# Optimization experiments

Measured on AMD Instinct MI355X. Metric: run time of the kernel, lower is better.

Reference implementation:

```python
import jax, jax.numpy as jnp
import numpy as np

OUT_H, OUT_W = 7, 7  # out_size from init_kwargs


def _split_coefficient(size, k):
    # Matches __split_coefficient: equal bins of round(size/k), last absorbs remainder.
    u = int(round(size / k))
    s = [u] * k
    s[-1] += size - k * u
    return s


def setup_inputs() -> dict:
    key = jax.random.key(0)
    x = jax.random.normal(key, (128, 57, 57, 512), dtype=jnp.float32)
    return {"x": x}


def reference(x) -> jnp.ndarray:
    # Adaptive max pooling over irregular static bins (NHWC -> [N, 7, 7, C]).
    N, H, W, C = x.shape
    h_s = _split_coefficient(H, OUT_H)
    w_s = _split_coefficient(W, OUT_W)
    h_off = np.cumsum([0] + h_s)  # static bin boundaries
    w_off = np.cumsum([0] + w_s)
    # Max over each H bin -> [N, OUT_H, W, C]
    rows = [x[:, h_off[i]:h_off[i + 1]].max(axis=1, keepdims=True) for i in range(OUT_H)]
    xh = jnp.concatenate(rows, axis=1)
    # Max over each W bin -> [N, OUT_H, OUT_W, C]
    cols = [xh[:, :, w_off[j]:w_off[j + 1]].max(axis=2, keepdims=True) for j in range(OUT_W)]
    return jnp.concatenate(cols, axis=2)
```

## Files before the change

### kernel.cpp

```cpp
#include <hip/hip_runtime.h>


#define N_  128
#define H_  57
#define W_  57
#define C_  512
#define OH_ 7
#define OW_ 7
#define C4_ (C_ / 4)

__global__ __launch_bounds__(128)
void adaptive_maxpool_kernel(const float* __restrict__ x, float* __restrict__ out) {
    const int bid = blockIdx.x;
    const int ow  = bid % OW_;
    const int oh  = (bid / OW_) % OH_;
    const int n   = bid / (OW_ * OH_);
    const int c4  = threadIdx.x;

    const int h0 = oh * 8;
    const int h1 = (oh == OH_ - 1) ? H_ : h0 + 8;
    const int w0 = ow * 8;
    const int w1 = (ow == OW_ - 1) ? W_ : w0 + 8;

    const float4* __restrict__ xin =
        reinterpret_cast<const float4*>(x) + (size_t)n * H_ * W_ * C4_ + c4;

    float4 m = make_float4(-INFINITY, -INFINITY, -INFINITY, -INFINITY);
    for (int h = h0; h < h1; ++h) {
        const float4* row = xin + (size_t)h * W_ * C4_ + (size_t)w0 * C4_;
        #pragma unroll 4
        for (int w = w0; w < w1; ++w) {
            float4 v = *row;
            row += C4_;
            m.x = fmaxf(m.x, v.x);
            m.y = fmaxf(m.y, v.y);
            m.z = fmaxf(m.z, v.z);
            m.w = fmaxf(m.w, v.w);
        }
    }

    float4* o = reinterpret_cast<float4*>(out) + (size_t)bid * C4_ + c4;
    *o = m;
}

extern "C" void kernel_launch(void* const* d_in, const int* in_sizes, int n_in,
                              void* d_out, int out_size, void* d_ws, size_t ws_size,
                              hipStream_t stream) {
    const float* x = (const float*)d_in[0];
    float* out = (float*)d_out;
    const int grid = N_ * OH_ * OW_;
    adaptive_maxpool_kernel<<<grid, 128, 0, stream>>>(x, out);
}
```

Measured before the change: 161.8 us.

## Process full width strip per block with split-row threads and LDS reduction

Each block now handles one (n, oh) row strip across all seven output columns instead of one output cell. The 256 threads form two groups that split the strip's rows in half, and the partial maxima are combined through shared memory before the output is written. Every thread issues a fully unrolled set of loads across the width, which raises memory-level parallelism per thread and cuts the block count by seven. The cost is more registers (seven float4 accumulators), a barrier, and fewer, larger blocks, which could limit occupancy.

```diff
diff --git a/kernel.cpp b/kernel.cpp
--- a/kernel.cpp
+++ b/kernel.cpp
@@ -1,46 +1,73 @@
 #include <hip/hip_runtime.h>
 
 
-#define N_  128
-#define H_  57
-#define W_  57
-#define C_  512
-#define OH_ 7
-#define OW_ 7
-#define C4_ (C_ / 4)
+#define N_   128
+#define H_   57
+#define W_   57
+#define C_   512
+#define OH_  7
+#define OW_  7
+#define C4_  (C_ / 4)
 
-__global__ __launch_bounds__(128)
-void adaptive_maxpool_kernel(const float* __restrict__ x, float* __restrict__ out) {
+__global__ __launch_bounds__(256)
+void adaptive_maxpool_strip(const float* __restrict__ x, float* __restrict__ out) {
     const int bid = blockIdx.x;
-    const int ow  = bid % OW_;
-    const int oh  = (bid / OW_) % OH_;
-    const int n   = bid / (OW_ * OH_);
-    const int c4  = threadIdx.x;
+    const int oh  = bid % OH_;
+    const int n   = bid / OH_;
+    const int c4  = threadIdx.x & (C4_ - 1);
+    const int g   = threadIdx.x >> 7;
 
-    const int h0 = oh * 8;
-    const int h1 = (oh == OH_ - 1) ? H_ : h0 + 8;
-    const int w0 = ow * 8;
-    const int w1 = (ow == OW_ - 1) ? W_ : w0 + 8;
+    const int h0  = oh * 8;
+    const int h1  = (oh == OH_ - 1) ? H_ : h0 + 8;
+    const int rh0 = g ? (h0 + 4) : h0;
+    const int rh1 = g ? h1 : (h0 + 4);
 
-    const float4* __restrict__ xin =
+    const float4* __restrict__ base =
         reinterpret_cast<const float4*>(x) + (size_t)n * H_ * W_ * C4_ + c4;
 
-    float4 m = make_float4(-INFINITY, -INFINITY, -INFINITY, -INFINITY);
-    for (int h = h0; h < h1; ++h) {
-        const float4* row = xin + (size_t)h * W_ * C4_ + (size_t)w0 * C4_;
-        #pragma unroll 4
-        for (int w = w0; w < w1; ++w) {
-            float4 v = *row;
-            row += C4_;
-            m.x = fmaxf(m.x, v.x);
-            m.y = fmaxf(m.y, v.y);
-            m.z = fmaxf(m.z, v.z);
-            m.w = fmaxf(m.w, v.w);
+    const float4 ninf = make_float4(-INFINITY, -INFINITY, -INFINITY, -INFINITY);
+    float4 acc[OW_];
+    #pragma unroll
+    for (int wb = 0; wb < OW_; ++wb) acc[wb] = ninf;
+
+    for (int h = rh0; h < rh1; ++h) {
+        const float4* __restrict__ row = base + (size_t)h * W_ * C4_;
+        #pragma unroll
+        for (int wb = 0; wb < OW_; ++wb) {
+            const int wcnt = (wb == OW_ - 1) ? 9 : 8;
+            #pragma unroll
+            for (int ww = 0; ww < 9; ++ww) {
+                if (ww < wcnt) {
+                    float4 v = row[(size_t)(wb * 8 + ww) * C4_];
+                    acc[wb].x = fmaxf(acc[wb].x, v.x);
+                    acc[wb].y = fmaxf(acc[wb].y, v.y);
+                    acc[wb].z = fmaxf(acc[wb].z, v.z);
+                    acc[wb].w = fmaxf(acc[wb].w, v.w);
+                }
+            }
         }
     }
 
-    float4* o = reinterpret_cast<float4*>(out) + (size_t)bid * C4_ + c4;
-    *o = m;
+    __shared__ float4 lds[OW_][C4_];
+    if (g == 1) {
+        #pragma unroll
+        for (int wb = 0; wb < OW_; ++wb) lds[wb][c4] = acc[wb];
+    }
+    __syncthreads();
+    if (g == 0) {
+        float4* __restrict__ o =
+            reinterpret_cast<float4*>(out) + (size_t)bid * OW_ * C4_ + c4;
+        #pragma unroll
+        for (int wb = 0; wb < OW_; ++wb) {
+            float4 p = lds[wb][c4];
+            float4 r;
+            r.x = fmaxf(acc[wb].x, p.x);
+            r.y = fmaxf(acc[wb].y, p.y);
+            r.z = fmaxf(acc[wb].z, p.z);
+            r.w = fmaxf(acc[wb].w, p.w);
+            o[(size_t)wb * C4_] = r;
+        }
+    }
 }
 
 extern "C" void kernel_launch(void* const* d_in, const int* in_sizes, int n_in,
@@ -48,6 +75,6 @@
                               hipStream_t stream) {
     const float* x = (const float*)d_in[0];
     float* out = (float*)d_out;
-    const int grid = N_ * OH_ * OW_;
-    adaptive_maxpool_kernel<<<grid, 128, 0, stream>>>(x, out);
+    const int grid = N_ * OH_;
+    adaptive_maxpool_strip<<<grid, 256, 0, stream>>>(x, out);
 }
```

New measurement: 166.2 us. +2.7%, slower.
